# Performance work log

Hardware: AMD Instinct MI355X
Metric: run time of the kernel (lower is better)

The kernel has to match this reference:

```python
import jax, jax.numpy as jnp
import numpy as np

B, S, E = 4, 2048, 1024


def setup_inputs() -> dict:
    key = jax.random.key(0)
    ks = jax.random.split(key, 7)
    s = 1.0 / np.sqrt(E)  # torch Linear default init scale (uniform bound)
    inp = {
        "input": jax.random.normal(ks[0], (B, S, E), dtype=jnp.float32),
        "masked": 1,
        "W_q": jax.random.uniform(ks[1], (E, E), jnp.float32, -s, s),
        "b_q": jax.random.uniform(ks[2], (E,), jnp.float32, -s, s),
        "W_k": jax.random.uniform(ks[3], (E, E), jnp.float32, -s, s),
        "b_k": jax.random.uniform(ks[4], (E,), jnp.float32, -s, s),
        "W_v": jax.random.uniform(ks[5], (E, E), jnp.float32, -s, s),
        "b_v": jax.random.uniform(ks[6], (E,), jnp.float32, -s, s),
    }
    return inp


def reference(input, masked, W_q, b_q, W_k, b_k, W_v, b_v):
    # torch.nn.Linear: y = x @ W.T + b
    q = jnp.einsum("bse,fe->bsf", input, W_q) + b_q
    k = jnp.einsum("bse,fe->bsf", input, W_k) + b_k
    v = jnp.einsum("bse,fe->bsf", input, W_v) + b_v
    d = q.shape[-1]
    scores = jnp.einsum("bqd,bkd->bqk", q, k) / jnp.sqrt(jnp.float32(d))
    if masked:
        Sq = scores.shape[1]
        causal = jnp.tril(jnp.ones((Sq, Sq), dtype=bool))  # [S,S], broadcast over batch
        scores = jnp.where(causal, scores, -jnp.inf)
    attn = jax.nn.softmax(scores, axis=-1)
    return jnp.einsum("bqk,bkd->bqd", attn, v)
```

## Files before the change

### kernel.cpp

```cpp
#include <hip/hip_runtime.h>

typedef _Float16 f16;
typedef f16 f16x8 __attribute__((ext_vector_type(8)));
typedef f16 f16x4v __attribute__((ext_vector_type(4)));
typedef f16 f16x2v __attribute__((ext_vector_type(2)));
typedef float f32x4 __attribute__((ext_vector_type(4)));

__device__ __forceinline__ void async_ld16(const void* g, void* l) {
    __builtin_amdgcn_global_load_lds(
        (const __attribute__((address_space(1))) unsigned int*)g,
        (__attribute__((address_space(3))) unsigned int*)l, 16, 0, 0);
}

#define VMC(n) asm volatile("s_waitcnt vmcnt(" #n ")" ::: "memory")
#define BAR __builtin_amdgcn_s_barrier()


#define STG(b, op, kh, P, P1, tOff) do {                                        \
    char* d_ = (char*)smem + (b) * 65536 + (op) * 32768 + (kh) * 16384 + stgBase; \
    async_ld16((P)  + (tOff) * 64 + (kh) * 32, d_);                             \
    async_ld16((P1) + (tOff) * 64 + (kh) * 32, d_ + 8192);                      \
} while (0)
#define RD_A(b, kk) do {                                                        \
    const char* s_ = (const char*)smem + (b) * 65536 + (kk) * 16384 + aOff;     \
    _Pragma("unroll") for (int m_ = 0; m_ < 8; ++m_)                            \
        af[m_] = *(const f16x8*)(s_ + m_ * 1024);                               \
} while (0)
#define RD_B2(b, kk, n0_) do {                                                  \
    const char* s_ = (const char*)smem + (b) * 65536 + 32768 + (kk) * 16384 + bOff; \
    bf[(n0_)]     = *(const f16x8*)(s_ + ((n0_)) * 1024);                       \
    bf[(n0_) + 1] = *(const f16x8*)(s_ + ((n0_) + 1) * 1024);                   \
} while (0)
#define FENCE_MM(n0_) do {                                                      \
    __builtin_amdgcn_s_barrier();                                               \
    asm volatile("s_waitcnt lgkmcnt(0)" ::: "memory");                          \
    __builtin_amdgcn_sched_barrier(0);                                          \
    __builtin_amdgcn_s_setprio(1);                                              \
    _Pragma("unroll") for (int m_ = 0; m_ < 8; ++m_) {                          \
        acc[m_][(n0_)]     = __builtin_amdgcn_mfma_f32_16x16x32_f16(af[m_], bf[(n0_)],     acc[m_][(n0_)],     0, 0, 0); \
        acc[m_][(n0_) + 1] = __builtin_amdgcn_mfma_f32_16x16x32_f16(af[m_], bf[(n0_) + 1], acc[m_][(n0_) + 1], 0, 0, 0); \
    }                                                                           \
    __builtin_amdgcn_s_setprio(0);                                              \
} while (0)

__global__ __launch_bounds__(512, 2) void scores256(
    const f16* __restrict__ Q, const f16* __restrict__ K,
    f16* __restrict__ P, const int* __restrict__ maskedp)
{
    const int masked = *maskedp;
    const int bx = blockIdx.x, by = blockIdx.y, bz = blockIdx.z;
    if (masked && bx > by) return;
    const int mBase = by * 256, nBase = bx * 256;

    __shared__ __align__(16) f16 smem[65536];
    const int tid = threadIdx.x;
    const int wave = tid >> 6, lane = tid & 63;
    const int wrow = wave >> 2, wcol = wave & 3;
    const int quad = lane >> 4, l16 = lane & 15;
    const int rowLane = tid >> 2;
    const int cOff = ((tid & 3) ^ ((tid >> 3) & 3)) * 8;
    const int stgBase = wave * 1024;
    const int swz  = (quad ^ ((l16 >> 1) & 3)) * 16;
    const int aOff = (wrow * 128 + l16) * 64 + swz;
    const int bOff = (wcol * 64 + l16) * 64 + swz;
    f32x4 acc[8][4];
#pragma unroll
    for (int m = 0; m < 8; ++m)
#pragma unroll
        for (int n = 0; n < 4; ++n) acc[m][n] = (f32x4){0.f, 0.f, 0.f, 0.f};
    f16x8 af[8], bf[4];

    const f16* Ab  = Q + (long)bz * (2048L * 1024);
    const f16* Btb = K + (long)bz * (2048L * 1024);
    const f16* pA  = Ab  + (long)(mBase + rowLane) * 1024 + cOff;
    const f16* pA1 = pA + 128 * 1024;
    const f16* pB  = Btb + (long)(nBase + rowLane) * 1024 + cOff;
    const f16* pB1 = pB + 128 * 1024;

    STG(0, 0, 0, pA, pA1, 0); STG(0, 1, 0, pB, pB1, 0);
    STG(0, 0, 1, pA, pA1, 0); STG(0, 1, 1, pB, pB1, 0);
    STG(1, 0, 0, pA, pA1, 1); STG(1, 1, 0, pB, pB1, 1);
    VMC(4);
    BAR;

#pragma unroll 1
    for (int i = 0; i < 7; ++i) {
        RD_A(0, 0); RD_B2(0, 0, 0); STG(1, 0, 1, pA, pA1, 1);
        FENCE_MM(0); BAR;
        RD_B2(0, 0, 2);             STG(1, 1, 1, pB, pB1, 1);
        FENCE_MM(2); BAR;
        RD_A(0, 1); RD_B2(0, 1, 0); STG(0, 0, 0, pA, pA1, 2);
        FENCE_MM(0); BAR;
        RD_B2(0, 1, 2);             STG(0, 1, 0, pB, pB1, 2);
        FENCE_MM(2); VMC(4); BAR;
        RD_A(1, 0); RD_B2(1, 0, 0); STG(0, 0, 1, pA, pA1, 2);
        FENCE_MM(0); BAR;
        RD_B2(1, 0, 2);             STG(0, 1, 1, pB, pB1, 2);
        FENCE_MM(2); BAR;
        RD_A(1, 1); RD_B2(1, 1, 0); STG(1, 0, 0, pA, pA1, 3);
        FENCE_MM(0); BAR;
        RD_B2(1, 1, 2);             STG(1, 1, 0, pB, pB1, 3);
        FENCE_MM(2); VMC(4); BAR;
        pA += 128; pA1 += 128; pB += 128; pB1 += 128;
    }
    RD_A(0, 0); RD_B2(0, 0, 0); STG(1, 0, 1, pA, pA1, 1);
    FENCE_MM(0); BAR;
    RD_B2(0, 0, 2);             STG(1, 1, 1, pB, pB1, 1);
    FENCE_MM(2); BAR;
    RD_A(0, 1); RD_B2(0, 1, 0);
    FENCE_MM(0); BAR;
    RD_B2(0, 1, 2);
    FENCE_MM(2); VMC(0); BAR;
    RD_A(1, 0); RD_B2(1, 0, 0);
    FENCE_MM(0); BAR;
    RD_B2(1, 0, 2);
    FENCE_MM(2); BAR;
    RD_A(1, 1); RD_B2(1, 1, 0);
    FENCE_MM(0); BAR;
    RD_B2(1, 1, 2);
    FENCE_MM(2);

    f16* Crow = P + (long)bz * (2048L * 2048);
#pragma unroll
    for (int m = 0; m < 8; ++m)
#pragma unroll
        for (int n = 0; n < 4; ++n)
#pragma unroll
            for (int r = 0; r < 4; ++r) {
                const int row = mBase + wrow * 128 + m * 16 + quad * 4 + r;
                const int col = nBase + wcol * 64 + n * 16 + l16;
                float e = __expf(acc[m][n][r] * 0.03125f);
                if (masked && col > row) e = 0.f;
                Crow[(long)row * 2048 + col] = (f16)e;
            }
}

#undef STG
#undef RD_A
#undef RD_B2
#undef FENCE_MM

#define QSTG_A(b, kh, tOff) do {                                                \
    char* d_ = (char*)smem + (b) * 49152 + (kh) * 8192 + stgBase;               \
    async_ld16(pA + (tOff) * 64 + (kh) * 32, d_);                               \
} while (0)
#define QSTG_B(b, kh, tOff) do {                                                \
    char* d_ = (char*)smem + (b) * 49152 + 16384 + (kh) * 16384 + stgBase;      \
    async_ld16(pB  + (tOff) * 64 + (kh) * 32, d_);                              \
    async_ld16(pB1 + (tOff) * 64 + (kh) * 32, d_ + 8192);                       \
} while (0)
#define QRD(b, kk) do {                                                         \
    const char* sa_ = (const char*)smem + (b) * 49152 + (kk) * 8192 + aOff;     \
    _Pragma("unroll") for (int m_ = 0; m_ < 4; ++m_)                            \
        af[m_] = *(const f16x8*)(sa_ + m_ * 1024);                              \
    const char* sb_ = (const char*)smem + (b) * 49152 + 16384 + (kk) * 16384 + bOff; \
    _Pragma("unroll") for (int n_ = 0; n_ < 4; ++n_)                            \
        bf[n_] = *(const f16x8*)(sb_ + n_ * 1024);                              \
} while (0)
#define QFENCE do {                                                             \
    __builtin_amdgcn_s_barrier();                                               \
    asm volatile("s_waitcnt lgkmcnt(0)" ::: "memory");                          \
    __builtin_amdgcn_sched_barrier(0);                                          \
    __builtin_amdgcn_s_setprio(1);                                              \
    _Pragma("unroll") for (int m_ = 0; m_ < 4; ++m_)                            \
        _Pragma("unroll") for (int n_ = 0; n_ < 4; ++n_)                        \
            acc[m_][n_] = __builtin_amdgcn_mfma_f32_16x16x32_f16(af[m_], bf[n_], acc[m_][n_], 0, 0, 0); \
    __builtin_amdgcn_s_setprio(0);                                              \
} while (0)

__global__ __launch_bounds__(512, 2) void qkv128(
    const f16* __restrict__ A, const f16* __restrict__ Bt,
    const float* __restrict__ b_q, const float* __restrict__ b_k,
    const float* __restrict__ b_v,
    f16* __restrict__ Q16, f16* __restrict__ K16, f16* __restrict__ Vt16)
{
    int bid = blockIdx.x;
    bid = (bid & 7) * 96 + (bid >> 3);
    const int by = bid / 12, bx = bid - by * 12;
    const int mBase = by * 128, nBase = bx * 256;

    __shared__ __align__(16) f16 smem[49152];
    const int tid = threadIdx.x;
    const int wave = tid >> 6, lane = tid & 63;
    const int wrow = wave >> 2, wcol = wave & 3;
    const int quad = lane >> 4, l16 = lane & 15;
    const int rowLane = tid >> 2;
    const int cOff = ((tid & 3) ^ ((tid >> 3) & 3)) * 8;
    const int stgBase = wave * 1024;
    const int swz  = (quad ^ ((l16 >> 1) & 3)) * 16;
    const int aOff = (wrow * 64 + l16) * 64 + swz;
    const int bOff = (wcol * 64 + l16) * 64 + swz;

    const f16* pA  = A  + (long)(mBase + rowLane) * 1024 + cOff;
    const f16* pB  = Bt + (long)(nBase + rowLane) * 1024 + cOff;
    const f16* pB1 = pB + 128 * 1024;

    f32x4 acc[4][4];
#pragma unroll
    for (int m = 0; m < 4; ++m)
#pragma unroll
        for (int n = 0; n < 4; ++n) acc[m][n] = (f32x4){0.f, 0.f, 0.f, 0.f};
    f16x8 af[4], bf[4];

    QSTG_A(0, 0, 0); QSTG_B(0, 0, 0);
    QSTG_A(0, 1, 0); QSTG_B(0, 1, 0);
    QSTG_A(1, 0, 1); QSTG_B(1, 0, 1);
    VMC(3);
    BAR;

#pragma unroll 1
    for (int i = 0; i < 7; ++i) {
        QRD(0, 0); QSTG_A(1, 1, 1); QSTG_B(1, 1, 1);
        QFENCE; VMC(6); BAR;
        QRD(0, 1); QSTG_A(0, 0, 2); QSTG_B(0, 0, 2);
        QFENCE; VMC(6); BAR;
        QRD(1, 0); QSTG_A(0, 1, 2); QSTG_B(0, 1, 2);
        QFENCE; VMC(6); BAR;
        QRD(1, 1); QSTG_A(1, 0, 3); QSTG_B(1, 0, 3);
        QFENCE; VMC(6); BAR;
        pA += 128; pB += 128; pB1 += 128;
    }
    QRD(0, 0); QSTG_A(1, 1, 1); QSTG_B(1, 1, 1);
    QFENCE; VMC(6); BAR;
    QRD(0, 1);
    QFENCE; VMC(3); BAR;
    QRD(1, 0);
    QFENCE; VMC(0); BAR;
    QRD(1, 1);
    QFENCE;
    BAR;

    const int seg = nBase >> 10;
    const float* bs = (seg == 0) ? b_q : (seg == 1) ? b_k : b_v;
    const int lcb = (nBase & 1023) + wcol * 64;
    float bvv[4];
#pragma unroll
    for (int n = 0; n < 4; ++n) bvv[n] = bs[lcb + n * 16 + l16];

    if (seg < 2) {
        f16* dst = (seg == 0) ? Q16 : K16;
#pragma unroll
        for (int m = 0; m < 4; ++m)
#pragma unroll
            for (int n = 0; n < 4; ++n)
#pragma unroll
                for (int r = 0; r < 4; ++r) {
                    const int row = mBase + wrow * 64 + m * 16 + quad * 4 + r;
                    dst[(long)row * 1024 + lcb + n * 16 + l16] =
                        (f16)(acc[m][n][r] + bvv[n]);
                }
    } else {
        const int b = mBase >> 11;
        const int s0 = (mBase & 2047) + wrow * 64;
        const int e0 = (nBase & 1023) + wcol * 64;
        f16* epiW = smem + wave * (64 * 72);
#pragma unroll
        for (int m = 0; m < 4; ++m)
#pragma unroll
            for (int n = 0; n < 4; ++n) {
                f16x4v pk;
#pragma unroll
                for (int r = 0; r < 4; ++r)
                    pk[r] = (f16)(acc[m][n][r] + bvv[n]);
                *(f16x4v*)&epiW[(n * 16 + l16) * 72 + m * 16 + quad * 4] = pk;
            }
        asm volatile("s_waitcnt lgkmcnt(0)" ::: "memory");
#pragma unroll
        for (int it = 0; it < 8; ++it) {
            const int e = it * 8 + (lane >> 3);
            const f16x8 v = *(const f16x8*)&epiW[e * 72 + (lane & 7) * 8];
            *(f16x8*)(Vt16 + ((long)b * 1024 + e0 + e) * 2048 + s0 +
                      (lane & 7) * 8) = v;
        }
    }
}

#undef QSTG_A
#undef QSTG_B
#undef QRD
#undef QFENCE

#if defined(__has_builtin)
#if __has_builtin(__builtin_amdgcn_fdot2)
#define HAVE_FDOT2 1
#endif
#endif

#ifdef HAVE_FDOT2
#define PSUM do {                                                               \
    const f16x2v one_ = {(f16)1, (f16)1};                                       \
    _Pragma("unroll") for (int m_ = 0; m_ < 4; ++m_) {                          \
        const f16x2v* ph_ = (const f16x2v*)&af[m_];                             \
        _Pragma("unroll") for (int j_ = 0; j_ < 4; ++j_)                        \
            rs[m_] = __builtin_amdgcn_fdot2(ph_[j_], one_, rs[m_], false);      \
    }                                                                           \
} while (0)
#else
#define PSUM do {                                                               \
    _Pragma("unroll") for (int m_ = 0; m_ < 4; ++m_)                            \
        _Pragma("unroll") for (int j_ = 0; j_ < 8; ++j_)                        \
            rs[m_] += (float)af[m_][j_];                                        \
} while (0)
#endif

#define PSTG_A(b, kh, tOff) do {                                                \
    char* d_ = (char*)smem + (b) * 32768 + (kh) * 8192 + stgBase;               \
    async_ld16(pA  + (tOff) * 64 + (kh) * 32, d_);                              \
    async_ld16(pA1 + (tOff) * 64 + (kh) * 32, d_ + 4096);                       \
} while (0)
#define PSTG_B(b, kh, tOff) do {                                                \
    char* d_ = (char*)smem + (b) * 32768 + 16384 + (kh) * 8192 + stgBase;       \
    async_ld16(pB  + (tOff) * 64 + (kh) * 32, d_);                              \
    async_ld16(pB1 + (tOff) * 64 + (kh) * 32, d_ + 4096);                       \
} while (0)
#define PRD(b, kk) do {                                                         \
    const char* sa_ = (const char*)smem + (b) * 32768 + (kk) * 8192 + aOff;     \
    _Pragma("unroll") for (int m_ = 0; m_ < 4; ++m_)                            \
        af[m_] = *(const f16x8*)(sa_ + m_ * 1024);                              \
    const char* sb_ = (const char*)smem + (b) * 32768 + 16384 + (kk) * 8192 + bOff; \
    _Pragma("unroll") for (int n_ = 0; n_ < 4; ++n_)                            \
        bf[n_] = *(const f16x8*)(sb_ + n_ * 1024);                              \
} while (0)
#define PFENCE do {                                                             \
    __builtin_amdgcn_s_barrier();                                               \
    asm volatile("s_waitcnt lgkmcnt(0)" ::: "memory");                          \
    __builtin_amdgcn_sched_barrier(0);                                          \
    __builtin_amdgcn_s_setprio(1);                                              \
    _Pragma("unroll") for (int m_ = 0; m_ < 4; ++m_)                            \
        _Pragma("unroll") for (int n_ = 0; n_ < 4; ++n_)                        \
            acc[m_][n_] = __builtin_amdgcn_mfma_f32_16x16x32_f16(af[m_], bf[n_], acc[m_][n_], 0, 0, 0); \
    __builtin_amdgcn_s_setprio(0);                                              \
    PSUM;                                                                       \
} while (0)

__global__ __launch_bounds__(256, 2) void pv128(
    const f16* __restrict__ P, const f16* __restrict__ Vt,
    float* __restrict__ out, const int* __restrict__ maskedp)
{
    const int masked = *maskedp;
    const int bx = blockIdx.x, bz = blockIdx.z;
    const int by = gridDim.y - 1 - blockIdx.y;
    const int mBase = by * 128, nBase = bx * 128;
    const int nIter = masked ? ((by >> 1) + 1) * 2 : 16;

    __shared__ __align__(16) f16 smem[32768];
    const int tid = threadIdx.x;
    const int wave = tid >> 6, lane = tid & 63;
    const int wrow = wave >> 1, wcol = wave & 1;
    const int quad = lane >> 4, l16 = lane & 15;
    const int rowLane = tid >> 2;
    const int cOff = ((tid & 3) ^ ((tid >> 3) & 3)) * 8;
    const int stgBase = wave * 1024;
    const int swz  = (quad ^ ((l16 >> 1) & 3)) * 16;
    const int aOff = (wrow * 64 + l16) * 64 + swz;
    const int bOff = (wcol * 64 + l16) * 64 + swz;

    const f16* Pb = P  + (long)bz * (2048L * 2048);
    const f16* Vb = Vt + (long)bz * (1024L * 2048);
    const f16* pA  = Pb + (long)(mBase + rowLane) * 2048 + cOff;
    const f16* pA1 = pA + 64 * 2048;
    const f16* pB  = Vb + (long)(nBase + rowLane) * 2048 + cOff;
    const f16* pB1 = pB + 64 * 2048;

    f32x4 acc[4][4];
#pragma unroll
    for (int m = 0; m < 4; ++m)
#pragma unroll
        for (int n = 0; n < 4; ++n) acc[m][n] = (f32x4){0.f, 0.f, 0.f, 0.f};
    f16x8 af[4], bf[4];
    float rs[4] = {0.f, 0.f, 0.f, 0.f};

    PSTG_A(0, 0, 0); PSTG_B(0, 0, 0);
    PSTG_A(0, 1, 0); PSTG_B(0, 1, 0);
    PSTG_A(1, 0, 1); PSTG_B(1, 0, 1);
    VMC(4);
    BAR;

#pragma unroll 1
    for (int i = 0; i < nIter - 1; ++i) {
        PRD(0, 0); PSTG_A(1, 1, 1); PSTG_B(1, 1, 1);
        PFENCE; VMC(8); BAR;
        PRD(0, 1); PSTG_A(0, 0, 2); PSTG_B(0, 0, 2);
        PFENCE; VMC(8); BAR;
        PRD(1, 0); PSTG_A(0, 1, 2); PSTG_B(0, 1, 2);
        PFENCE; VMC(8); BAR;
        PRD(1, 1); PSTG_A(1, 0, 3); PSTG_B(1, 0, 3);
        PFENCE; VMC(8); BAR;
        pA += 128; pA1 += 128; pB += 128; pB1 += 128;
    }
    PRD(0, 0); PSTG_A(1, 1, 1); PSTG_B(1, 1, 1);
    PFENCE; VMC(8); BAR;
    PRD(0, 1);
    PFENCE; VMC(4); BAR;
    PRD(1, 0);
    PFENCE; VMC(0); BAR;
    PRD(1, 1);
    PFENCE;

#pragma unroll
    for (int m = 0; m < 4; ++m) {
        rs[m] += __shfl_xor(rs[m], 16);
        rs[m] += __shfl_xor(rs[m], 32);
    }

    float* ob = out + (long)bz * (2048L * 1024);
#pragma unroll
    for (int m = 0; m < 4; ++m)
#pragma unroll
        for (int r = 0; r < 4; ++r) {
            const int row = mBase + wrow * 64 + m * 16 + quad * 4 + r;
            const float inv = 1.f / __shfl(rs[m], quad * 4 + r);
#pragma unroll
            for (int n = 0; n < 4; ++n) {
                const int col = nBase + wcol * 64 + n * 16 + l16;
                ob[(long)row * 1024 + col] = acc[m][n][r] * inv;
            }
        }
}

#undef PSTG_A
#undef PSTG_B
#undef PRD
#undef PFENCE
#undef PSUM
#undef VMC
#undef BAR

__global__ void cvt_all(const float* __restrict__ inp,
                        const float* __restrict__ W0,
                        const float* __restrict__ W1,
                        const float* __restrict__ W2,
                        f16* __restrict__ inp16, f16* __restrict__ W3)
{
    const int bxx = blockIdx.x;
    const float* src;
    f16* dst;
    int i;
    if (bxx < 8192) {
        src = inp; dst = inp16;
        i = bxx * 256 + threadIdx.x;
    } else {
        const int wb = bxx - 8192;
        const int which = wb >> 10;
        src = (which == 0) ? W0 : (which == 1) ? W1 : W2;
        dst = W3 + (long)which * 1024 * 1024;
        i = (wb & 1023) * 256 + threadIdx.x;
    }
    const float4 v = ((const float4*)src)[i];
    f16x4v o;
    o[0] = (f16)v.x; o[1] = (f16)v.y; o[2] = (f16)v.z; o[3] = (f16)v.w;
    ((f16x4v*)dst)[i] = o;
}

extern "C" void kernel_launch(void* const* d_in, const int* in_sizes, int n_in,
                              void* d_out, int out_size, void* d_ws, size_t ws_size,
                              hipStream_t stream)
{
    const float* inp = (const float*)d_in[0];
    const int* masked = (const int*)d_in[1];
    const float* Wq = (const float*)d_in[2];
    const float* bq = (const float*)d_in[3];
    const float* Wk = (const float*)d_in[4];
    const float* bk = (const float*)d_in[5];
    const float* Wv = (const float*)d_in[6];
    const float* bv = (const float*)d_in[7];
    float* out = (float*)d_out;

    const int S = 2048, E = 1024;
    const long nTok = (long)4 * S;

    char* ws = (char*)d_ws;
    f16* inp16 = (f16*)ws;   ws += nTok * E * 2;
    f16* W3    = (f16*)ws;   ws += (long)3 * E * E * 2;
    f16* Q16   = (f16*)ws;   ws += nTok * E * 2;
    f16* K16   = (f16*)ws;   ws += nTok * E * 2;
    f16* Vt16  = (f16*)ws;   ws += nTok * E * 2;
    f16* P16   = (f16*)ws;   ws += (long)4 * S * S * 2;

    cvt_all<<<dim3(8192 + 3072), dim3(256), 0, stream>>>(
        inp, Wq, Wk, Wv, inp16, W3);

    qkv128<<<dim3(768), dim3(512), 0, stream>>>(
        inp16, W3, bq, bk, bv, Q16, K16, Vt16);

    scores256<<<dim3(8, 8, 4), dim3(512), 0, stream>>>(
        Q16, K16, P16, masked);

    pv128<<<dim3(8, 16, 4), dim3(256), 0, stream>>>(
        P16, Vt16, out, masked);
}
```

Before: 241.2 us.

## Triple-buffer QKV GEMM shared-memory pipeline and alternate PV tile order per batch

The QKV projection kernel moves from a double-buffered to a triple-buffered LDS pipeline. Shared memory grows from 96KB to 144KB, and loads are issued two k-tiles ahead, with vmcnt waits only every other phase. This is meant to hide more global-load latency behind MFMA work. With 512-thread blocks and launch bounds of 2, the larger LDS footprint may cut residency to one block per CU. Separately, the PV kernel reverses the row-block order for batches 2 and above so that long and short causal tiles mix across the grid, which should balance the workload.

```diff
diff --git a/kernel.cpp b/kernel.cpp
--- a/kernel.cpp
+++ b/kernel.cpp
@@ -14,7 +14,6 @@
 
 #define VMC(n) asm volatile("s_waitcnt vmcnt(" #n ")" ::: "memory")
 #define BAR __builtin_amdgcn_s_barrier()
-
 
 #define STG(b, op, kh, P, P1, tOff) do {                                        \
     char* d_ = (char*)smem + (b) * 65536 + (op) * 32768 + (kh) * 16384 + stgBase; \
@@ -140,20 +139,20 @@
 #undef RD_B2
 #undef FENCE_MM
 
-#define QSTG_A(b, kh, tOff) do {                                                \
-    char* d_ = (char*)smem + (b) * 49152 + (kh) * 8192 + stgBase;               \
+#define QSTG_A3(b, kh, tOff) do {                                               \
+    char* d_ = (char*)smem + (b) * 16384 + (kh) * 8192 + wave * 1024;           \
     async_ld16(pA + (tOff) * 64 + (kh) * 32, d_);                               \
 } while (0)
-#define QSTG_B(b, kh, tOff) do {                                                \
-    char* d_ = (char*)smem + (b) * 49152 + 16384 + (kh) * 16384 + stgBase;      \
+#define QSTG_B3(b, kh, tOff) do {                                               \
+    char* d_ = (char*)smem + 49152 + (b) * 32768 + (kh) * 16384 + wave * 1024;  \
     async_ld16(pB  + (tOff) * 64 + (kh) * 32, d_);                              \
     async_ld16(pB1 + (tOff) * 64 + (kh) * 32, d_ + 8192);                       \
 } while (0)
-#define QRD(b, kk) do {                                                         \
-    const char* sa_ = (const char*)smem + (b) * 49152 + (kk) * 8192 + aOff;     \
+#define QRD3(b, kk) do {                                                        \
+    const char* sa_ = (const char*)smem + (b) * 16384 + (kk) * 8192 + aOff;     \
     _Pragma("unroll") for (int m_ = 0; m_ < 4; ++m_)                            \
         af[m_] = *(const f16x8*)(sa_ + m_ * 1024);                              \
-    const char* sb_ = (const char*)smem + (b) * 49152 + 16384 + (kk) * 16384 + bOff; \
+    const char* sb_ = (const char*)smem + 49152 + (b) * 32768 + (kk) * 16384 + bOff; \
     _Pragma("unroll") for (int n_ = 0; n_ < 4; ++n_)                            \
         bf[n_] = *(const f16x8*)(sb_ + n_ * 1024);                              \
 } while (0)
@@ -167,6 +166,10 @@
             acc[m_][n_] = __builtin_amdgcn_mfma_f32_16x16x32_f16(af[m_], bf[n_], acc[m_][n_], 0, 0, 0); \
     __builtin_amdgcn_s_setprio(0);                                              \
 } while (0)
+#define QP0(b, b2, o2) do { QRD3(b, 0); QSTG_A3(b2, 1, o2); QSTG_B3(b2, 1, o2); \
+    QFENCE; BAR; } while (0)
+#define QP1(b, o3) do { QRD3(b, 1); QSTG_A3(b, 0, o3); QSTG_B3(b, 0, o3);       \
+    QFENCE; VMC(9); BAR; } while (0)
 
 __global__ __launch_bounds__(512, 2) void qkv128(
     const f16* __restrict__ A, const f16* __restrict__ Bt,
@@ -179,14 +182,13 @@
     const int by = bid / 12, bx = bid - by * 12;
     const int mBase = by * 128, nBase = bx * 256;
 
-    __shared__ __align__(16) f16 smem[49152];
+    __shared__ __align__(16) f16 smem[73728];
     const int tid = threadIdx.x;
     const int wave = tid >> 6, lane = tid & 63;
     const int wrow = wave >> 2, wcol = wave & 3;
     const int quad = lane >> 4, l16 = lane & 15;
     const int rowLane = tid >> 2;
     const int cOff = ((tid & 3) ^ ((tid >> 3) & 3)) * 8;
-    const int stgBase = wave * 1024;
     const int swz  = (quad ^ ((l16 >> 1) & 3)) * 16;
     const int aOff = (wrow * 64 + l16) * 64 + swz;
     const int bOff = (wcol * 64 + l16) * 64 + swz;
@@ -202,31 +204,33 @@
         for (int n = 0; n < 4; ++n) acc[m][n] = (f32x4){0.f, 0.f, 0.f, 0.f};
     f16x8 af[4], bf[4];
 
-    QSTG_A(0, 0, 0); QSTG_B(0, 0, 0);
-    QSTG_A(0, 1, 0); QSTG_B(0, 1, 0);
-    QSTG_A(1, 0, 1); QSTG_B(1, 0, 1);
-    VMC(3);
+    QSTG_A3(0, 0, 0); QSTG_B3(0, 0, 0);
+    QSTG_A3(0, 1, 0); QSTG_B3(0, 1, 0);
+    QSTG_A3(1, 0, 1); QSTG_B3(1, 0, 1);
+    QSTG_A3(1, 1, 1); QSTG_B3(1, 1, 1);
+    QSTG_A3(2, 0, 2); QSTG_B3(2, 0, 2);
+    VMC(9);
     BAR;
 
 #pragma unroll 1
-    for (int i = 0; i < 7; ++i) {
-        QRD(0, 0); QSTG_A(1, 1, 1); QSTG_B(1, 1, 1);
-        QFENCE; VMC(6); BAR;
-        QRD(0, 1); QSTG_A(0, 0, 2); QSTG_B(0, 0, 2);
-        QFENCE; VMC(6); BAR;
-        QRD(1, 0); QSTG_A(0, 1, 2); QSTG_B(0, 1, 2);
-        QFENCE; VMC(6); BAR;
-        QRD(1, 1); QSTG_A(1, 0, 3); QSTG_B(1, 0, 3);
-        QFENCE; VMC(6); BAR;
-        pA += 128; pB += 128; pB1 += 128;
-    }
-    QRD(0, 0); QSTG_A(1, 1, 1); QSTG_B(1, 1, 1);
+    for (int g = 0; g < 4; ++g) {
+        QP0(0, 2, 2); QP1(0, 3);
+        QP0(1, 0, 3); QP1(1, 4);
+        QP0(2, 1, 4); QP1(2, 5);
+        pA += 192; pB += 192; pB1 += 192;
+    }
+    QP0(0, 2, 2); QP1(0, 3);
+    QRD3(1, 0); QSTG_A3(0, 1, 3); QSTG_B3(0, 1, 3);
+    QFENCE; BAR;
+    QRD3(1, 1);
     QFENCE; VMC(6); BAR;
-    QRD(0, 1);
-    QFENCE; VMC(3); BAR;
-    QRD(1, 0);
+    QRD3(2, 0);
+    QFENCE; BAR;
+    QRD3(2, 1);
     QFENCE; VMC(0); BAR;
-    QRD(1, 1);
+    QRD3(0, 0);
+    QFENCE; BAR;
+    QRD3(0, 1);
     QFENCE;
     BAR;
 
@@ -275,10 +279,12 @@
     }
 }
 
-#undef QSTG_A
-#undef QSTG_B
-#undef QRD
+#undef QSTG_A3
+#undef QSTG_B3
+#undef QRD3
 #undef QFENCE
+#undef QP0
+#undef QP1
 
 #if defined(__has_builtin)
 #if __has_builtin(__builtin_amdgcn_fdot2)
@@ -339,7 +345,7 @@
 {
     const int masked = *maskedp;
     const int bx = blockIdx.x, bz = blockIdx.z;
-    const int by = gridDim.y - 1 - blockIdx.y;
+    const int by = (bz >= 2) ? blockIdx.y : (gridDim.y - 1 - blockIdx.y);
     const int mBase = by * 128, nBase = bx * 128;
     const int nIter = masked ? ((by >> 1) + 1) * 2 : 16;
 
```

Measured after the change: 235.2 us. -2.5%, faster.
